# Kernel tuning notes

Hardware: AMD Instinct MI355X
Metric: run time of the kernel (lower is better)

Reference implementation:

```python
import jax, jax.numpy as jnp
import numpy as np

B, T, D = 32, 1024, 512  # batch, max_X (sequence), encoder width (== rnn width)
H = 10                   # hidden units of first attention Dense


def setup_inputs() -> dict:
    key = jax.random.key(0)
    k1, k2, k3, k4 = jax.random.split(key, 4)
    return {
        "cbhg_encoding": jax.random.normal(k1, (B, T, D), dtype=jnp.float32),
        "attention_rnn_output": jax.random.normal(k2, (B, D), dtype=jnp.float32),
        "W1": jax.random.normal(k3, (2 * D, H), dtype=jnp.float32) * (1.0 / np.sqrt(2 * D)),
        "b1": jnp.zeros((H,), dtype=jnp.float32),
        "W2": jax.random.normal(k4, (H, 1), dtype=jnp.float32) * (1.0 / np.sqrt(H)),
        "b2": jnp.zeros((1,), dtype=jnp.float32),
    }


def reference(cbhg_encoding, attention_rnn_output, W1, b1, W2, b2):
    b, t, d = cbhg_encoding.shape
    # RepeatVector(max_X): [B, D] -> [B, T, D]
    rnn_rep = jnp.broadcast_to(attention_rnn_output[:, None, :], (b, t, d))
    # Concatenate(axis=-1): [B, T, 2D]
    attn_in = jnp.concatenate([cbhg_encoding, rnn_rep], axis=-1)
    # Dense(10, tanh) -> Dense(1, relu): energies [B, T, 1]
    e = jnp.tanh(jnp.einsum("btf,fh->bth", attn_in, W1) + b1)
    energies = jax.nn.relu(jnp.einsum("bth,ho->bto", e, W2) + b2)
    # softmax over the sequence axis (attention weights over T)
    attention_weights = jax.nn.softmax(energies, axis=1)  # [B, T, 1]
    # Dot(axes=1): contract sequence axis -> context [B, 1, D]
    context = jnp.einsum("bti,btd->bid", attention_weights, cbhg_encoding)
    # Reshape rnn output to match context shape [B, 1, D]
    rnn_reshaped = attention_rnn_output.reshape(b, 1, d)
    return (context, rnn_reshaped)
```

## Files before the change

kernel.cpp:

```cpp
#include <hip/hip_runtime.h>

#define BB 32
#define TT 1024
#define DD 512
#define HH 10


__global__ __launch_bounds__(256) void k0_init(
    const float* __restrict__ rnn, const float* __restrict__ W1,
    const float* __restrict__ b1, float* __restrict__ out,
    float* __restrict__ cbh) {
  const int b = blockIdx.x;
  const int tid = threadIdx.x;

  const float r0 = rnn[b * DD + tid];
  const float r1 = rnn[b * DD + tid + 256];

  out[b * DD + tid] = 0.f;
  out[b * DD + tid + 256] = 0.f;
  out[BB * DD + b * DD + tid] = r0;
  out[BB * DD + b * DD + tid + 256] = r1;

  float s[HH];
#pragma unroll
  for (int h = 0; h < HH; ++h) {
    s[h] = r0 * W1[(DD + tid) * HH + h] + r1 * W1[(DD + tid + 256) * HH + h];
  }

  __shared__ float red[256][HH];
#pragma unroll
  for (int h = 0; h < HH; ++h) red[tid][h] = s[h];
  __syncthreads();
  for (int off = 128; off > 0; off >>= 1) {
    if (tid < off) {
#pragma unroll
      for (int h = 0; h < HH; ++h) red[tid][h] += red[tid + off][h];
    }
    __syncthreads();
  }
  if (tid < HH) cbh[b * HH + tid] = red[0][tid] + b1[tid];
}

__global__ __launch_bounds__(256, 4) void kA_energies(
    const float* __restrict__ x, const float* __restrict__ W1,
    const float* __restrict__ cbh, const float* __restrict__ W2,
    const float* __restrict__ b2, float* __restrict__ E) {
  const int lane = threadIdx.x & 63;
  const int wid = blockIdx.x * (blockDim.x >> 6) + (threadIdx.x >> 6);
  const int f0 = lane * 4;

  float wA[4][HH], wB[4][HH];
#pragma unroll
  for (int k = 0; k < 4; ++k) {
#pragma unroll
    for (int h = 0; h < HH; ++h) {
      wA[k][h] = W1[(f0 + k) * HH + h];
      wB[k][h] = W1[(256 + f0 + k) * HH + h];
    }
  }
  float w2r[HH];
#pragma unroll
  for (int h = 0; h < HH; ++h) w2r[h] = W2[h];
  const float b2v = b2[0];

  const int NW = 4096;
  for (int row = wid; row < BB * TT; row += NW) {
    const float4 x0 = *reinterpret_cast<const float4*>(x + row * DD + f0);
    const float4 x1 = *reinterpret_cast<const float4*>(x + row * DD + 256 + f0);

    float s[HH];
#pragma unroll
    for (int h = 0; h < HH; ++h) {
      float v = x0.x * wA[0][h];
      v = fmaf(x0.y, wA[1][h], v);
      v = fmaf(x0.z, wA[2][h], v);
      v = fmaf(x0.w, wA[3][h], v);
      v = fmaf(x1.x, wB[0][h], v);
      v = fmaf(x1.y, wB[1][h], v);
      v = fmaf(x1.z, wB[2][h], v);
      v = fmaf(x1.w, wB[3][h], v);
      s[h] = v;
    }
#pragma unroll
    for (int h = 0; h < HH; ++h) {
      float v = s[h];
#pragma unroll
      for (int off = 32; off > 0; off >>= 1) v += __shfl_xor(v, off, 64);
      s[h] = v;
    }
    const int b = row >> 10;
    float e = b2v;
#pragma unroll
    for (int h = 0; h < HH; ++h) {
      const float v = s[h] + cbh[b * HH + h];
      const float z = __expf(2.f * v);
      const float th = 1.f - 2.f * __builtin_amdgcn_rcpf(z + 1.f);
      e = fmaf(th, w2r[h], e);
    }
    if (lane == 0) E[row] = fmaxf(e, 0.f);
  }
}

__global__ __launch_bounds__(256) void kB_context(
    const float* __restrict__ x, const float* __restrict__ E,
    float* __restrict__ out) {
  const int tid = threadIdx.x;
  const int b = blockIdx.x >> 4;
  const int tc = blockIdx.x & 15;

  __shared__ float we[TT];
  __shared__ float red[256];

  const float4 e4 = *reinterpret_cast<const float4*>(E + b * TT + tid * 4);
  float m = fmaxf(fmaxf(e4.x, e4.y), fmaxf(e4.z, e4.w));
  red[tid] = m;
  __syncthreads();
  for (int off = 128; off > 0; off >>= 1) {
    if (tid < off) red[tid] = fmaxf(red[tid], red[tid + off]);
    __syncthreads();
  }
  const float mx = red[0];
  __syncthreads();

  const float w0 = __expf(e4.x - mx);
  const float w1 = __expf(e4.y - mx);
  const float w2 = __expf(e4.z - mx);
  const float w3 = __expf(e4.w - mx);
  we[tid * 4 + 0] = w0;
  we[tid * 4 + 1] = w1;
  we[tid * 4 + 2] = w2;
  we[tid * 4 + 3] = w3;
  red[tid] = w0 + w1 + w2 + w3;
  __syncthreads();
  for (int off = 128; off > 0; off >>= 1) {
    if (tid < off) red[tid] += red[tid + off];
    __syncthreads();
  }
  const float rs = 1.f / red[0];

  const float* xb = x + (size_t)(b * TT + tc * 64) * DD;
  float ax = 0.f, ay = 0.f;
#pragma unroll 4
  for (int i = 0; i < 64; ++i) {
    const float w = we[tc * 64 + i];
    const float2 xv = *reinterpret_cast<const float2*>(xb + i * DD + tid * 2);
    ax = fmaf(w, xv.x, ax);
    ay = fmaf(w, xv.y, ay);
  }
  atomicAdd(out + b * DD + tid * 2 + 0, ax * rs);
  atomicAdd(out + b * DD + tid * 2 + 1, ay * rs);
}

extern "C" void kernel_launch(void* const* d_in, const int* in_sizes, int n_in,
                              void* d_out, int out_size, void* d_ws,
                              size_t ws_size, hipStream_t stream) {
  const float* cbhg = (const float*)d_in[0];
  const float* rnn = (const float*)d_in[1];
  const float* W1 = (const float*)d_in[2];
  const float* b1 = (const float*)d_in[3];
  const float* W2 = (const float*)d_in[4];
  const float* b2 = (const float*)d_in[5];
  float* out = (float*)d_out;

  float* E = (float*)d_ws;
  float* cbh = E + BB * TT;

  k0_init<<<BB, 256, 0, stream>>>(rnn, W1, b1, out, cbh);
  kA_energies<<<1024, 256, 0, stream>>>(cbhg, W1, cbh, W2, b2, E);
  kB_context<<<BB * 16, 256, 0, stream>>>(cbhg, E, out);
}
```

Baseline: 131.3 us.

## Fuse energy and context passes per chunk, drop max-subtraction and atomics

```diff
diff --git a/kernel.cpp b/kernel.cpp
--- a/kernel.cpp
+++ b/kernel.cpp
@@ -4,28 +4,35 @@
 #define TT 1024
 #define DD 512
 #define HH 10
+#define WP 12
+#define CHUNK 64
+#define NCH (TT / CHUNK)
 
 
 __global__ __launch_bounds__(256) void k0_init(
     const float* __restrict__ rnn, const float* __restrict__ W1,
     const float* __restrict__ b1, float* __restrict__ out,
-    float* __restrict__ cbh) {
+    float* __restrict__ cbh, float* __restrict__ wpad) {
   const int b = blockIdx.x;
   const int tid = threadIdx.x;
 
   const float r0 = rnn[b * DD + tid];
   const float r1 = rnn[b * DD + tid + 256];
 
-  out[b * DD + tid] = 0.f;
-  out[b * DD + tid + 256] = 0.f;
   out[BB * DD + b * DD + tid] = r0;
   out[BB * DD + b * DD + tid + 256] = r1;
 
+  if (tid < 16 * WP) {
+    const int idx = b * 16 * WP + tid;
+    const int f = idx / WP;
+    const int h = idx % WP;
+    wpad[idx] = (h < HH) ? W1[f * HH + h] : 0.f;
+  }
+
   float s[HH];
 #pragma unroll
-  for (int h = 0; h < HH; ++h) {
+  for (int h = 0; h < HH; ++h)
     s[h] = r0 * W1[(DD + tid) * HH + h] + r1 * W1[(DD + tid + 256) * HH + h];
-  }
 
   __shared__ float red[256][HH];
 #pragma unroll
@@ -41,114 +48,106 @@
   if (tid < HH) cbh[b * HH + tid] = red[0][tid] + b1[tid];
 }
 
-__global__ __launch_bounds__(256, 4) void kA_energies(
-    const float* __restrict__ x, const float* __restrict__ W1,
+__global__ __launch_bounds__(256, 2) void k1_fused(
+    const float* __restrict__ x, const float* __restrict__ wpad,
     const float* __restrict__ cbh, const float* __restrict__ W2,
-    const float* __restrict__ b2, float* __restrict__ E) {
+    const float* __restrict__ b2, float* __restrict__ pc,
+    float* __restrict__ sc) {
+  const int b = blockIdx.x >> 4;
+  const int tc = blockIdx.x & 15;
   const int lane = threadIdx.x & 63;
-  const int wid = blockIdx.x * (blockDim.x >> 6) + (threadIdx.x >> 6);
-  const int f0 = lane * 4;
+  const int wv = __builtin_amdgcn_readfirstlane(threadIdx.x >> 6);
 
-  float wA[4][HH], wB[4][HH];
+  __shared__ float hpart[4][CHUNK][13];
+  __shared__ float wgt[CHUNK];
+
+  const int row = b * TT + tc * CHUNK + lane;
+  const float* xr = x + (size_t)row * DD + wv * 128;
+  const float* wp = wpad + wv * 128 * WP;
+
+  float acc[HH];
 #pragma unroll
-  for (int k = 0; k < 4; ++k) {
+  for (int h = 0; h < HH; ++h) acc[h] = 0.f;
+
+#pragma unroll 4
+  for (int k = 0; k < 32; ++k) {
+    const float4 xv = *reinterpret_cast<const float4*>(xr + k * 4);
+    const float xa[4] = {xv.x, xv.y, xv.z, xv.w};
+#pragma unroll
+    for (int j = 0; j < 4; ++j) {
+      const float4 wa = *reinterpret_cast<const float4*>(wp + (k * 4 + j) * WP);
+      const float4 wb = *reinterpret_cast<const float4*>(wp + (k * 4 + j) * WP + 4);
+      const float2 wc = *reinterpret_cast<const float2*>(wp + (k * 4 + j) * WP + 8);
+      const float xs = xa[j];
+      acc[0] = fmaf(xs, wa.x, acc[0]);
+      acc[1] = fmaf(xs, wa.y, acc[1]);
+      acc[2] = fmaf(xs, wa.z, acc[2]);
+      acc[3] = fmaf(xs, wa.w, acc[3]);
+      acc[4] = fmaf(xs, wb.x, acc[4]);
+      acc[5] = fmaf(xs, wb.y, acc[5]);
+      acc[6] = fmaf(xs, wb.z, acc[6]);
+      acc[7] = fmaf(xs, wb.w, acc[7]);
+      acc[8] = fmaf(xs, wc.x, acc[8]);
+      acc[9] = fmaf(xs, wc.y, acc[9]);
+    }
+  }
+
+#pragma unroll
+  for (int h = 0; h < HH; ++h) hpart[wv][lane][h] = acc[h];
+  __syncthreads();
+
+  if (threadIdx.x < 64) {
+    float e = b2[0];
 #pragma unroll
     for (int h = 0; h < HH; ++h) {
-      wA[k][h] = W1[(f0 + k) * HH + h];
-      wB[k][h] = W1[(256 + f0 + k) * HH + h];
+      const float v = hpart[0][lane][h] + hpart[1][lane][h] +
+                      hpart[2][lane][h] + hpart[3][lane][h] + cbh[b * HH + h];
+      const float z = __expf(2.f * v);
+      const float th = 1.f - 2.f / (z + 1.f);
+      e = fmaf(th, W2[h], e);
     }
+    float w = __expf(fmaxf(e, 0.f));
+    wgt[lane] = w;
+#pragma unroll
+    for (int off = 32; off > 0; off >>= 1) w += __shfl_xor(w, off, 64);
+    if (lane == 0) sc[b * NCH + tc] = w;
   }
-  float w2r[HH];
-#pragma unroll
-  for (int h = 0; h < HH; ++h) w2r[h] = W2[h];
-  const float b2v = b2[0];
+  __syncthreads();
 
-  const int NW = 4096;
-  for (int row = wid; row < BB * TT; row += NW) {
-    const float4 x0 = *reinterpret_cast<const float4*>(x + row * DD + f0);
-    const float4 x1 = *reinterpret_cast<const float4*>(x + row * DD + 256 + f0);
-
-    float s[HH];
-#pragma unroll
-    for (int h = 0; h < HH; ++h) {
-      float v = x0.x * wA[0][h];
-      v = fmaf(x0.y, wA[1][h], v);
-      v = fmaf(x0.z, wA[2][h], v);
-      v = fmaf(x0.w, wA[3][h], v);
-      v = fmaf(x1.x, wB[0][h], v);
-      v = fmaf(x1.y, wB[1][h], v);
-      v = fmaf(x1.z, wB[2][h], v);
-      v = fmaf(x1.w, wB[3][h], v);
-      s[h] = v;
-    }
-#pragma unroll
-    for (int h = 0; h < HH; ++h) {
-      float v = s[h];
-#pragma unroll
-      for (int off = 32; off > 0; off >>= 1) v += __shfl_xor(v, off, 64);
-      s[h] = v;
-    }
-    const int b = row >> 10;
-    float e = b2v;
-#pragma unroll
-    for (int h = 0; h < HH; ++h) {
-      const float v = s[h] + cbh[b * HH + h];
-      const float z = __expf(2.f * v);
-      const float th = 1.f - 2.f * __builtin_amdgcn_rcpf(z + 1.f);
-      e = fmaf(th, w2r[h], e);
-    }
-    if (lane == 0) E[row] = fmaxf(e, 0.f);
+  const int d0 = threadIdx.x * 2;
+  const float* xb = x + (size_t)(b * TT + tc * CHUNK) * DD + d0;
+  float ax = 0.f, ay = 0.f;
+#pragma unroll 8
+  for (int r = 0; r < CHUNK; ++r) {
+    const float wr = wgt[r];
+    const float2 xv = *reinterpret_cast<const float2*>(xb + (size_t)r * DD);
+    ax = fmaf(wr, xv.x, ax);
+    ay = fmaf(wr, xv.y, ay);
   }
+  *reinterpret_cast<float2*>(pc + (size_t)(b * NCH + tc) * DD + d0) =
+      make_float2(ax, ay);
 }
 
-__global__ __launch_bounds__(256) void kB_context(
-    const float* __restrict__ x, const float* __restrict__ E,
+__global__ __launch_bounds__(256) void k2_combine(
+    const float* __restrict__ pc, const float* __restrict__ sc,
     float* __restrict__ out) {
-  const int tid = threadIdx.x;
-  const int b = blockIdx.x >> 4;
-  const int tc = blockIdx.x & 15;
+  const int b = blockIdx.x;
+  const int d0 = threadIdx.x * 2;
 
-  __shared__ float we[TT];
-  __shared__ float red[256];
+  float ssum = 0.f;
+#pragma unroll
+  for (int c = 0; c < NCH; ++c) ssum += sc[b * NCH + c];
 
-  const float4 e4 = *reinterpret_cast<const float4*>(E + b * TT + tid * 4);
-  float m = fmaxf(fmaxf(e4.x, e4.y), fmaxf(e4.z, e4.w));
-  red[tid] = m;
-  __syncthreads();
-  for (int off = 128; off > 0; off >>= 1) {
-    if (tid < off) red[tid] = fmaxf(red[tid], red[tid + off]);
-    __syncthreads();
+  float ax = 0.f, ay = 0.f;
+#pragma unroll
+  for (int c = 0; c < NCH; ++c) {
+    const float2 v =
+        *reinterpret_cast<const float2*>(pc + (size_t)(b * NCH + c) * DD + d0);
+    ax += v.x;
+    ay += v.y;
   }
-  const float mx = red[0];
-  __syncthreads();
-
-  const float w0 = __expf(e4.x - mx);
-  const float w1 = __expf(e4.y - mx);
-  const float w2 = __expf(e4.z - mx);
-  const float w3 = __expf(e4.w - mx);
-  we[tid * 4 + 0] = w0;
-  we[tid * 4 + 1] = w1;
-  we[tid * 4 + 2] = w2;
-  we[tid * 4 + 3] = w3;
-  red[tid] = w0 + w1 + w2 + w3;
-  __syncthreads();
-  for (int off = 128; off > 0; off >>= 1) {
-    if (tid < off) red[tid] += red[tid + off];
-    __syncthreads();
-  }
-  const float rs = 1.f / red[0];
-
-  const float* xb = x + (size_t)(b * TT + tc * 64) * DD;
-  float ax = 0.f, ay = 0.f;
-#pragma unroll 4
-  for (int i = 0; i < 64; ++i) {
-    const float w = we[tc * 64 + i];
-    const float2 xv = *reinterpret_cast<const float2*>(xb + i * DD + tid * 2);
-    ax = fmaf(w, xv.x, ax);
-    ay = fmaf(w, xv.y, ay);
-  }
-  atomicAdd(out + b * DD + tid * 2 + 0, ax * rs);
-  atomicAdd(out + b * DD + tid * 2 + 1, ay * rs);
+  const float inv = 1.f / ssum;
+  *reinterpret_cast<float2*>(out + b * DD + d0) = make_float2(ax * inv, ay * inv);
 }
 
 extern "C" void kernel_launch(void* const* d_in, const int* in_sizes, int n_in,
@@ -162,10 +161,12 @@
   const float* b2 = (const float*)d_in[5];
   float* out = (float*)d_out;
 
-  float* E = (float*)d_ws;
-  float* cbh = E + BB * TT;
+  float* wpad = (float*)d_ws;
+  float* cbh = wpad + DD * WP;
+  float* pc = wpad + 6656;
+  float* sc = pc + BB * NCH * DD;
 
-  k0_init<<<BB, 256, 0, stream>>>(rnn, W1, b1, out, cbh);
-  kA_energies<<<1024, 256, 0, stream>>>(cbhg, W1, cbh, W2, b2, E);
-  kB_context<<<BB * 16, 256, 0, stream>>>(cbhg, E, out);
+  k0_init<<<BB, 256, 0, stream>>>(rnn, W1, b1, out, cbh, wpad);
+  k1_fused<<<BB * NCH, 256, 0, stream>>>(cbhg, wpad, cbh, W2, b2, pc, sc);
+  k2_combine<<<BB, 256, 0, stream>>>(pc, sc, out);
 }
```

Measured after the change: 117.9 us. 10.2% less time.
